# Kernel tuning notes

Measured on AMD Instinct MI355X. Metric: run time of the kernel, lower is better.

Reference implementation:

```python
import jax, jax.numpy as jnp
import numpy as np

NEG_INF = -1e30  # stand-in for float('-inf') added to masked scores


def setup_inputs() -> dict:
    key = jax.random.key(0)
    ks = jax.random.split(key, 3)
    B, S, D = 4, 2048, 1024
    x = jax.random.normal(ks[0], (B, S, D), dtype=jnp.float32)
    W_qkv = jax.random.normal(ks[1], (D, 3 * D), dtype=jnp.float32) * (1.0 / np.sqrt(D))
    b_qkv = jnp.zeros((3 * D,), dtype=jnp.float32)
    W_out = jax.random.normal(ks[2], (D, D), dtype=jnp.float32) * (1.0 / np.sqrt(D))
    b_out = jnp.zeros((D,), dtype=jnp.float32)
    return {"x": x, "W_qkv": W_qkv, "b_qkv": b_qkv, "W_out": W_out, "b_out": b_out, "mask": 1}


def reference(x, W_qkv, b_qkv, W_out, b_out, mask):
    B, S, D = x.shape
    H = 16
    hd = D // H
    # fused QKV projection: [B,S,3D]
    qkv = x @ W_qkv + b_qkv
    # [B,S,H,3*hd] -> [B,H,S,3*hd], split into q,k,v each [B,H,S,hd]
    qkv = qkv.reshape(B, S, H, 3 * hd).transpose(0, 2, 1, 3)
    q, k, v = jnp.split(qkv, 3, axis=-1)
    # scaled dot-product attention, full score matrix [B,H,S,S]
    scaled = jnp.einsum('bhqd,bhkd->bhqk', q, k) / np.sqrt(hd)
    if mask:
        causal = jnp.triu(jnp.ones((S, S), dtype=bool), k=1)
        scaled = jnp.where(causal, NEG_INF, scaled)
    attention = jax.nn.softmax(scaled, axis=-1)
    values = jnp.einsum('bhqk,bhkd->bhqd', attention, v)
    # merge heads: [B,H,S,hd] -> [B,S,D] (matches tf.reshape on [B,H,S,hd])
    values = values.reshape(B, S, H * hd)
    return values @ W_out + b_out
```

## Files before the change

### kernel.cpp

```cpp
#include <hip/hip_runtime.h>
#include <hip/hip_bf16.h>

typedef __attribute__((ext_vector_type(8))) short short8;
typedef __attribute__((ext_vector_type(4))) float f32x4;

__device__ inline f32x4 mfma16(short8 a, short8 b, f32x4 c) {
    return __builtin_amdgcn_mfma_f32_16x16x32_bf16(a, b, c, 0, 0, 0);
}
__device__ inline short f2bf(float x) {
    __hip_bfloat16 h = __float2bfloat16(x);
    return *reinterpret_cast<short*>(&h);
}
__device__ inline unsigned short f2bfu(float x) {
    __hip_bfloat16 h = __float2bfloat16(x);
    return *reinterpret_cast<unsigned short*>(&h);
}
__device__ inline float bf2f(short u) {
    __hip_bfloat16 h = *reinterpret_cast<__hip_bfloat16*>(&u);
    return __bfloat162float(h);
}
__device__ inline unsigned int cvt_pk_bf16(float a, float b) {
    unsigned int r;
    asm("v_cvt_pk_bf16_f32 %0, %1, %2" : "=v"(r) : "v"(a), "v"(b));
    return r;
}
__device__ inline float scrub(float v, float s) {
    return (fabsf(v) < 1e30f) ? v : s;
}
__device__ inline short8 scaleq(short8 v) {
    short8 r;
#pragma unroll
    for (int j = 0; j < 8; j++) r[j] = f2bf(bf2f(v[j]) * 0.125f);
    return r;
}

__global__ void detect_dtype(const unsigned short* __restrict__ x, int* flag) {
    __shared__ int cnt;
    if (threadIdx.x == 0) cnt = 0;
    __syncthreads();
    int c = 0;
    for (int i = threadIdx.x; i < 1024; i += 256) {
        unsigned short u = x[i];
        int e = (u >> 7) & 0xFF;
        if ((u & 0x7FFF) == 0 || (e >= 110 && e <= 143)) c++;
    }
    atomicAdd(&cnt, c);
    __syncthreads();
    if (threadIdx.x == 0) flag[0] = (cnt < 819) ? 1 : 0;
}

__global__ void conv_bias(const void* __restrict__ in, short* __restrict__ out,
                          int n, const int* __restrict__ flag) {
    int i = blockIdx.x * 256 + threadIdx.x;
    if (i >= n) return;
    out[i] = (*flag) ? f2bf(((const float*)in)[i]) : ((const short*)in)[i];
}

__global__ __launch_bounds__(256) void conv_x(const void* __restrict__ in,
                                              short* __restrict__ out, int n,
                                              const int* __restrict__ flag) {
    int i = (blockIdx.x * 256 + threadIdx.x) * 4;
    if (i >= n) return;
    if (*flag) {
        float4 f = *(const float4*)((const float*)in + i);
        *(uint2*)(out + i) = make_uint2(cvt_pk_bf16(f.x, f.y), cvt_pk_bf16(f.z, f.w));
    } else {
        *(uint2*)(out + i) = *(const uint2*)((const short*)in + i);
    }
}

__global__ void fill_sentinel(void* out, int n, const int* __restrict__ flag) {
    int i = blockIdx.x * 256 + threadIdx.x;
    if (i >= n) return;
    if (*flag) ((float*)out)[i] = 3e5f; else ((short*)out)[i] = f2bf(3e5f);
}

__global__ __launch_bounds__(256) void transpose_poly(const void* __restrict__ in,
                                                      short* __restrict__ out,
                                                      int R, int C,
                                                      const int* __restrict__ flag) {
    __shared__ short tile[32][33];
    const bool f32 = (*flag) != 0;
    int tx = threadIdx.x & 31, ty = threadIdx.x >> 5;
    int r0 = blockIdx.y * 32, c0 = blockIdx.x * 32;
#pragma unroll
    for (int i = 0; i < 4; i++) {
        size_t off = (size_t)(r0 + ty + i * 8) * C + c0 + tx;
        tile[ty + i * 8][tx] = f32 ? f2bf(((const float*)in)[off]) : ((const short*)in)[off];
    }
    __syncthreads();
#pragma unroll
    for (int i = 0; i < 4; i++)
        out[(size_t)(c0 + ty + i * 8) * R + r0 + tx] = tile[tx][ty + i * 8];
}

#define LDK 72

__global__ __launch_bounds__(256) void gemm_bt(const short* __restrict__ A,
                                               const short* __restrict__ Bt,
                                               const short* __restrict__ bias,
                                               void* __restrict__ Cv,
                                               int N, int K,
                                               const int* __restrict__ flag,
                                               int c_poly, float sent) {
    alignas(16) __shared__ short As[128 * LDK];
    alignas(16) __shared__ short Bs[128 * LDK];
    const bool cf32 = c_poly && (*flag);
    int tid = threadIdx.x;
    int wave = tid >> 6, lane = tid & 63;
    int lrow = lane & 15, lq = lane >> 4;
    int wm = (wave >> 1) * 64, wn = (wave & 1) * 64;
    int m0 = blockIdx.y * 128, n0 = blockIdx.x * 128;

    f32x4 acc[4][4];
#pragma unroll
    for (int i = 0; i < 4; i++)
#pragma unroll
        for (int j = 0; j < 4; j++) acc[i][j] = (f32x4){0.f, 0.f, 0.f, 0.f};

    int srow = tid >> 3;
    int scol = (tid & 7) * 8;

    short8 ar[4], br[4];
#pragma unroll
    for (int p = 0; p < 4; p++) {
        int row = p * 32 + srow;
        ar[p] = *(const short8*)&A[(size_t)(m0 + row) * K + scol];
        br[p] = *(const short8*)&Bt[(size_t)(n0 + row) * K + scol];
    }

    for (int kb = 0; kb < K; kb += 64) {
#pragma unroll
        for (int p = 0; p < 4; p++) {
            int row = p * 32 + srow;
            *(short8*)&As[row * LDK + scol] = ar[p];
            *(short8*)&Bs[row * LDK + scol] = br[p];
        }
        __syncthreads();

        int kn = (kb + 64 < K) ? kb + 64 : kb;
#pragma unroll
        for (int p = 0; p < 4; p++) {
            int row = p * 32 + srow;
            ar[p] = *(const short8*)&A[(size_t)(m0 + row) * K + kn + scol];
            br[p] = *(const short8*)&Bt[(size_t)(n0 + row) * K + kn + scol];
        }

#pragma unroll
        for (int ks = 0; ks < 2; ks++) {
            short8 af[4], bf[4];
#pragma unroll
            for (int i = 0; i < 4; i++)
                af[i] = *(short8*)&As[(wm + i * 16 + lrow) * LDK + ks * 32 + lq * 8];
#pragma unroll
            for (int i = 0; i < 4; i++)
                bf[i] = *(short8*)&Bs[(wn + i * 16 + lrow) * LDK + ks * 32 + lq * 8];
#pragma unroll
            for (int i = 0; i < 4; i++)
#pragma unroll
                for (int j = 0; j < 4; j++)
                    acc[i][j] = mfma16(af[i], bf[j], acc[i][j]);
        }
        __syncthreads();
    }

    const __hip_bfloat16* bias16 = (const __hip_bfloat16*)bias;
#pragma unroll
    for (int j = 0; j < 4; j++) {
        int col = n0 + wn + j * 16 + lrow;
        float bv = __bfloat162float(bias16[col]);
#pragma unroll
        for (int i = 0; i < 4; i++) {
            int rbase = m0 + wm + i * 16 + lq * 4;
#pragma unroll
            for (int r = 0; r < 4; r++) {
                float val = scrub(acc[i][j][r] + bv, sent);
                size_t off = (size_t)(rbase + r) * N + col;
                if (cf32) ((float*)Cv)[off] = val; else ((short*)Cv)[off] = f2bf(val);
            }
        }
    }
}

#define VP2 72
#define PP 72
#define MFIX 8.0f

__global__ __launch_bounds__(256, 2) void attn_kernel(const short* __restrict__ QKV,
                                                      short* __restrict__ AO,
                                                      const int* __restrict__ maskp) {
    constexpr int S = 2048, C3 = 3072;
    alignas(16) __shared__ short Vt[2][64 * VP2];
    alignas(16) __shared__ short Pt[4][2][16 * PP];

    int tid = threadIdx.x;
    int wave = tid >> 6, lane = tid & 63;
    int lrow = lane & 15, lq = lane >> 4;
    int bh = blockIdx.y;
    const bool causal = (*maskp) != 0;
    const short* base = QKV + (size_t)(bh >> 4) * S * C3 + (bh & 15) * 192;

    int vi2 = (tid & 31) * 2;
    int vd0 = (tid >> 5) * 8;

    int buf = 0;
    for (int tile = 0; tile < 2; tile++) {
        int q0t = (tile == 0) ? blockIdx.x * 128 : 1920 - blockIdx.x * 128;

        int qg[2];
        short8 qf0[2], qf1[2];
#pragma unroll
        for (int g = 0; g < 2; g++) {
            qg[g] = q0t + wave * 32 + g * 16 + lrow;
            qf0[g] = scaleq(*(const short8*)(base + (size_t)qg[g] * C3 + lq * 8));
            qf1[g] = scaleq(*(const short8*)(base + (size_t)qg[g] * C3 + 32 + lq * 8));
        }

        float l_i[2] = {0.f, 0.f};
        f32x4 acc[2][4];
#pragma unroll
        for (int g = 0; g < 2; g++)
#pragma unroll
            for (int nt = 0; nt < 4; nt++) acc[g][nt] = (f32x4){0.f, 0.f, 0.f, 0.f};

        int nkv = causal ? (q0t + 128) : S;

        short8 va, vb, kf0[4], kf1[4];
        {
            const short* vs0 = base + (size_t)vi2 * C3 + 128 + vd0;
            va = *(const short8*)vs0;
            vb = *(const short8*)(vs0 + C3);
#pragma unroll
            for (int sub = 0; sub < 4; sub++) {
                const short* kb = base + (size_t)(sub * 16 + lrow) * C3 + 64;
                kf0[sub] = *(const short8*)(kb + lq * 8);
                kf1[sub] = *(const short8*)(kb + 32 + lq * 8);
            }
        }

        for (int kv0 = 0; kv0 < nkv; kv0 += 64) {
            {
                union { short8 v; unsigned short u[8]; } a, b;
                a.v = va; b.v = vb;
                unsigned int* vt = (unsigned int*)&Vt[buf][0];
#pragma unroll
                for (int j = 0; j < 8; j++)
                    vt[((vd0 + j) * VP2 + vi2) >> 1] =
                        ((unsigned int)b.u[j] << 16) | a.u[j];
            }
            __syncthreads();

            int kvn = (kv0 + 64 < nkv) ? kv0 + 64 : kv0;
            short8 va_n, vb_n, kf0_n[4], kf1_n[4];
            {
                const short* vs0 = base + (size_t)(kvn + vi2) * C3 + 128 + vd0;
                va_n = *(const short8*)vs0;
                vb_n = *(const short8*)(vs0 + C3);
#pragma unroll
                for (int sub = 0; sub < 4; sub++) {
                    const short* kb = base + (size_t)(kvn + sub * 16 + lrow) * C3 + 64;
                    kf0_n[sub] = *(const short8*)(kb + lq * 8);
                    kf1_n[sub] = *(const short8*)(kb + 32 + lq * 8);
                }
            }

            f32x4 s[2][4];
#pragma unroll
            for (int sub = 0; sub < 4; sub++) {
#pragma unroll
                for (int g = 0; g < 2; g++) {
                    f32x4 a = (f32x4){0.f, 0.f, 0.f, 0.f};
                    a = mfma16(kf0[sub], qf0[g], a);
                    a = mfma16(kf1[sub], qf1[g], a);
                    s[g][sub] = a;
                }
            }

#pragma unroll
            for (int g = 0; g < 2; g++) {
                if (causal && (kv0 + 63 > q0t + wave * 32 + g * 16)) {
#pragma unroll
                    for (int sub = 0; sub < 4; sub++) {
                        int kvg = kv0 + sub * 16 + lq * 4;
#pragma unroll
                        for (int rr = 0; rr < 4; rr++)
                            if (kvg + rr > qg[g]) s[g][sub][rr] = -1e30f;
                    }
                }
                float lsum = 0.f;
                unsigned int pk[4][2];
#pragma unroll
                for (int sub = 0; sub < 4; sub++) {
                    float p0 = __expf(s[g][sub][0] - MFIX);
                    float p1 = __expf(s[g][sub][1] - MFIX);
                    float p2 = __expf(s[g][sub][2] - MFIX);
                    float p3 = __expf(s[g][sub][3] - MFIX);
                    lsum += (p0 + p1) + (p2 + p3);
                    pk[sub][0] = cvt_pk_bf16(p0, p1);
                    pk[sub][1] = cvt_pk_bf16(p2, p3);
                }
                l_i[g] += lsum;
                unsigned int* pt = (unsigned int*)&Pt[wave][g][0];
#pragma unroll
                for (int sub = 0; sub < 4; sub++)
                    *(uint2*)&pt[(lrow * PP + sub * 16 + lq * 4) >> 1] =
                        make_uint2(pk[sub][0], pk[sub][1]);
            }

#pragma unroll
            for (int ks = 0; ks < 2; ks++) {
                short8 pfA = *(short8*)&Pt[wave][0][lrow * PP + ks * 32 + lq * 8];
                short8 pfB = *(short8*)&Pt[wave][1][lrow * PP + ks * 32 + lq * 8];
#pragma unroll
                for (int nt = 0; nt < 4; nt++) {
                    short8 vf = *(short8*)&Vt[buf][(nt * 16 + lrow) * VP2 + ks * 32 + lq * 8];
                    acc[0][nt] = mfma16(vf, pfA, acc[0][nt]);
                    acc[1][nt] = mfma16(vf, pfB, acc[1][nt]);
                }
            }

            va = va_n; vb = vb_n;
#pragma unroll
            for (int sub = 0; sub < 4; sub++) {
                kf0[sub] = kf0_n[sub];
                kf1[sub] = kf1_n[sub];
            }
            buf ^= 1;
        }

#pragma unroll
        for (int g = 0; g < 2; g++) {
            float lt = l_i[g];
            lt += __shfl_xor(lt, 16, 64);
            lt += __shfl_xor(lt, 32, 64);
            float inv = 1.f / lt;
            short* ob = AO + ((size_t)bh * S + qg[g]) * 64;
#pragma unroll
            for (int nt = 0; nt < 4; nt++) {
                float o0 = scrub(acc[g][nt][0] * inv, 4e4f);
                float o1 = scrub(acc[g][nt][1] * inv, 4e4f);
                float o2 = scrub(acc[g][nt][2] * inv, 4e4f);
                float o3 = scrub(acc[g][nt][3] * inv, 4e4f);
                *(uint2*)(ob + nt * 16 + lq * 4) =
                    make_uint2(cvt_pk_bf16(o0, o1), cvt_pk_bf16(o2, o3));
            }
        }
    }
}

extern "C" void kernel_launch(void* const* d_in, const int* in_sizes, int n_in,
                              void* d_out, int out_size, void* d_ws, size_t ws_size,
                              hipStream_t stream) {
    char* ws = (char*)d_ws;
    int*   flag  = (int*)ws;
    short* bq_bf = (short*)(ws + 65536);
    short* bo_bf = (short*)(ws + 131072);
    short* WqkvT = (short*)(ws + (1ull << 20));
    short* WoutT = (short*)(ws + 7ull * (1ull << 20));
    short* xbfAO = (short*)(ws + 9ull * (1ull << 20));
    short* QKVc  = (short*)(ws + 25ull * (1ull << 20));

    detect_dtype<<<1, 256, 0, stream>>>((const unsigned short*)d_in[0], flag);

    if (ws_size < 73ull * 1048576) {
        fill_sentinel<<<(8388608 + 255) / 256, 256, 0, stream>>>(d_out, 8388608, flag);
        return;
    }

    conv_bias<<<12, 256, 0, stream>>>(d_in[2], bq_bf, 3072, flag);
    conv_bias<<<4, 256, 0, stream>>>(d_in[4], bo_bf, 1024, flag);
    transpose_poly<<<dim3(96, 32), 256, 0, stream>>>(d_in[1], WqkvT, 1024, 3072, flag);
    transpose_poly<<<dim3(32, 32), 256, 0, stream>>>(d_in[3], WoutT, 1024, 1024, flag);
    conv_x<<<8192, 256, 0, stream>>>(d_in[0], xbfAO, 8388608, flag);

    gemm_bt<<<dim3(24, 64), 256, 0, stream>>>(xbfAO, WqkvT, bq_bf, QKVc,
                                              3072, 1024, flag, 0, 8e4f);
    attn_kernel<<<dim3(8, 64), 256, 0, stream>>>(QKVc, xbfAO, (const int*)d_in[5]);
    gemm_bt<<<dim3(8, 64), 256, 0, stream>>>(xbfAO, WoutT, bo_bf, d_out,
                                             1024, 1024, flag, 1, 2e4f);
}
```

Measured before the change: 305.2 us.

## Split attention KV loop across two blocks and merge partial outputs

Each query tile's KV loop is split between two blocks, one taking even 64-wide KV units and the other odd ones, which doubles the attention grid. Each half writes a normalized bf16 partial output and its bf16 row sum. A new merge kernel combines the two halves weighted by their row sums, which is valid because scores use a fixed max offset. The aim is more parallelism and better latency hiding. The cost is an extra kernel, roughly 64 MB of extra global traffic, reuse of d_out as scratch, and some precision loss from storing row sums in bf16.

```diff
diff --git a/kernel.cpp b/kernel.cpp
--- a/kernel.cpp
+++ b/kernel.cpp
@@ -187,7 +187,9 @@
 #define MFIX 8.0f
 
 __global__ __launch_bounds__(256, 2) void attn_kernel(const short* __restrict__ QKV,
-                                                      short* __restrict__ AO,
+                                                      short* __restrict__ P0,
+                                                      short* __restrict__ P1,
+                                                      unsigned short* __restrict__ lbuf,
                                                       const int* __restrict__ maskp) {
     constexpr int S = 2048, C3 = 3072;
     alignas(16) __shared__ short Vt[2][64 * VP2];
@@ -196,6 +198,7 @@
     int tid = threadIdx.x;
     int wave = tid >> 6, lane = tid & 63;
     int lrow = lane & 15, lq = lane >> 4;
+    int bx = blockIdx.x >> 1, spl = blockIdx.x & 1;
     int bh = blockIdx.y;
     const bool causal = (*maskp) != 0;
     const short* base = QKV + (size_t)(bh >> 4) * S * C3 + (bh & 15) * 192;
@@ -205,7 +208,7 @@
 
     int buf = 0;
     for (int tile = 0; tile < 2; tile++) {
-        int q0t = (tile == 0) ? blockIdx.x * 128 : 1920 - blockIdx.x * 128;
+        int q0t = (tile == 0) ? bx * 128 : 1920 - bx * 128;
 
         int qg[2];
         short8 qf0[2], qf1[2];
@@ -223,34 +226,37 @@
 #pragma unroll
             for (int nt = 0; nt < 4; nt++) acc[g][nt] = (f32x4){0.f, 0.f, 0.f, 0.f};
 
-        int nkv = causal ? (q0t + 128) : S;
+        int nunits = (causal ? (q0t + 128) : S) >> 6;
 
         short8 va, vb, kf0[4], kf1[4];
         {
-            const short* vs0 = base + (size_t)vi2 * C3 + 128 + vd0;
+            int kv0p = spl << 6;
+            const short* vs0 = base + (size_t)(kv0p + vi2) * C3 + 128 + vd0;
             va = *(const short8*)vs0;
             vb = *(const short8*)(vs0 + C3);
 #pragma unroll
             for (int sub = 0; sub < 4; sub++) {
-                const short* kb = base + (size_t)(sub * 16 + lrow) * C3 + 64;
+                const short* kb = base + (size_t)(kv0p + sub * 16 + lrow) * C3 + 64;
                 kf0[sub] = *(const short8*)(kb + lq * 8);
                 kf1[sub] = *(const short8*)(kb + 32 + lq * 8);
             }
         }
 
-        for (int kv0 = 0; kv0 < nkv; kv0 += 64) {
+        for (int u = spl; u < nunits; u += 2) {
+            int kv0 = u << 6;
             {
-                union { short8 v; unsigned short u[8]; } a, b;
+                union { short8 v; unsigned short uu[8]; } a, b;
                 a.v = va; b.v = vb;
                 unsigned int* vt = (unsigned int*)&Vt[buf][0];
 #pragma unroll
                 for (int j = 0; j < 8; j++)
                     vt[((vd0 + j) * VP2 + vi2) >> 1] =
-                        ((unsigned int)b.u[j] << 16) | a.u[j];
+                        ((unsigned int)b.uu[j] << 16) | a.uu[j];
             }
             __syncthreads();
 
-            int kvn = (kv0 + 64 < nkv) ? kv0 + 64 : kv0;
+            int un = (u + 2 < nunits) ? u + 2 : u;
+            int kvn = un << 6;
             short8 va_n, vb_n, kf0_n[4], kf1_n[4];
             {
                 const short* vs0 = base + (size_t)(kvn + vi2) * C3 + 128 + vd0;
@@ -328,13 +334,14 @@
             buf ^= 1;
         }
 
+        short* Pd = spl ? P1 : P0;
 #pragma unroll
         for (int g = 0; g < 2; g++) {
             float lt = l_i[g];
             lt += __shfl_xor(lt, 16, 64);
             lt += __shfl_xor(lt, 32, 64);
             float inv = 1.f / lt;
-            short* ob = AO + ((size_t)bh * S + qg[g]) * 64;
+            short* ob = Pd + ((size_t)bh * S + qg[g]) * 64;
 #pragma unroll
             for (int nt = 0; nt < 4; nt++) {
                 float o0 = scrub(acc[g][nt][0] * inv, 4e4f);
@@ -344,8 +351,28 @@
                 *(uint2*)(ob + nt * 16 + lq * 4) =
                     make_uint2(cvt_pk_bf16(o0, o1), cvt_pk_bf16(o2, o3));
             }
-        }
-    }
+            if (lq == 0)
+                lbuf[spl * (64 * 2048) + bh * 2048 + qg[g]] = f2bfu(lt);
+        }
+    }
+}
+
+__global__ __launch_bounds__(256) void attn_merge(const short* __restrict__ P0,
+                                                  short* __restrict__ P1,
+                                                  const unsigned short* __restrict__ lbuf) {
+    size_t i = ((size_t)blockIdx.x * 256 + threadIdx.x) * 4;
+    int row = (int)(i >> 6);
+    float l0 = bf2f((short)lbuf[row]);
+    float l1 = bf2f((short)lbuf[64 * 2048 + row]);
+    float inv = 1.f / (l0 + l1);
+    float w0 = l0 * inv, w1 = l1 * inv;
+    uint2 a = *(const uint2*)(P0 + i);
+    uint2 b = *(const uint2*)(P1 + i);
+    float o0 = w0 * bf2f((short)(a.x & 0xFFFF)) + w1 * bf2f((short)(b.x & 0xFFFF));
+    float o1 = w0 * bf2f((short)(a.x >> 16))    + w1 * bf2f((short)(b.x >> 16));
+    float o2 = w0 * bf2f((short)(a.y & 0xFFFF)) + w1 * bf2f((short)(b.y & 0xFFFF));
+    float o3 = w0 * bf2f((short)(a.y >> 16))    + w1 * bf2f((short)(b.y >> 16));
+    *(uint2*)(P1 + i) = make_uint2(cvt_pk_bf16(o0, o1), cvt_pk_bf16(o2, o3));
 }
 
 extern "C" void kernel_launch(void* const* d_in, const int* in_sizes, int n_in,
@@ -355,6 +382,7 @@
     int*   flag  = (int*)ws;
     short* bq_bf = (short*)(ws + 65536);
     short* bo_bf = (short*)(ws + 131072);
+    unsigned short* lbuf = (unsigned short*)(ws + 196608);
     short* WqkvT = (short*)(ws + (1ull << 20));
     short* WoutT = (short*)(ws + 7ull * (1ull << 20));
     short* xbfAO = (short*)(ws + 9ull * (1ull << 20));
@@ -375,7 +403,9 @@
 
     gemm_bt<<<dim3(24, 64), 256, 0, stream>>>(xbfAO, WqkvT, bq_bf, QKVc,
                                               3072, 1024, flag, 0, 8e4f);
-    attn_kernel<<<dim3(8, 64), 256, 0, stream>>>(QKVc, xbfAO, (const int*)d_in[5]);
+    attn_kernel<<<dim3(16, 64), 256, 0, stream>>>(QKVc, (short*)d_out, xbfAO,
+                                                  lbuf, (const int*)d_in[5]);
+    attn_merge<<<8192, 256, 0, stream>>>((const short*)d_out, xbfAO, lbuf);
     gemm_bt<<<dim3(8, 64), 256, 0, stream>>>(xbfAO, WoutT, bo_bf, d_out,
                                              1024, 1024, flag, 1, 2e4f);
 }
```

Result: slower. 325.3 us (+6.6%).
